# Performance work log

Hardware: AMD Instinct MI355X
Metric: run time of the kernel (lower is better)

The kernel has to match this reference:

```python
import jax, jax.numpy as jnp
import numpy as np

H, D, L, G = 4, 32, 2, 512   # heads, head_dim, conv layers, num graphs
HC = H * D                    # hidden_channels = 128


def _mlp3(x, ws, bs):
    # PyG-style MLP, 3 layers, relu between (no act after last), dropout=0
    for i in range(3):
        x = x @ ws[i] + bs[i]
        if i < 2:
            x = jax.nn.relu(x)
    return x


def _attend(q_dst, k_src, v_src, edge, a_rel_et, m_rel_et, p_rel_et, n_dst):
    """One HGTConv edge-type: relation transform, per-dst segment softmax, scatter.
    q_dst: [Nd,H,D], k_src/v_src: [Ns,H,D], edge: [2,E] (src,dst)."""
    src, dst = edge[0], edge[1]
    k_t = jnp.einsum('nhd,hde->nhe', k_src, a_rel_et)   # relation-specific key
    v_t = jnp.einsum('nhd,hde->nhe', v_src, m_rel_et)   # relation-specific value
    alpha = (q_dst[dst] * k_t[src]).sum(-1) * p_rel_et / jnp.sqrt(jnp.float32(D))  # [E,H]
    amax = jax.ops.segment_max(alpha, dst, num_segments=n_dst)
    amax = jnp.where(jnp.isfinite(amax), amax, 0.0)      # nodes with no in-edges
    ex = jnp.exp(alpha - amax[dst])
    den = jax.ops.segment_sum(ex, dst, num_segments=n_dst)
    w = ex / den[dst]                                    # segment softmax weights
    out = jax.ops.segment_sum(v_t[src] * w[..., None], dst, num_segments=n_dst)
    return out.reshape(n_dst, HC)


def _forward(x_var, x_con, mlp_in_w, mlp_in_b,
             mlp_out_w0, mlp_out_b0, mlp_out_w1, mlp_out_b1, mlp_out_w2, mlp_out_b2,
             k_w, k_b, q_w, q_b, v_w, v_b, a_w, a_b, skip,
             a_rel, m_rel, p_rel, edge_vc, edge_cv, batch_var):
    Nv, Nc = x_var.shape[0], x_con.shape[0]
    # per-node-type input MLPs (nt 0 = variable, nt 1 = constraint)
    xs = [_mlp3(x_var, mlp_in_w[0], mlp_in_b[0]),
          _mlp3(x_con, mlp_in_w[1], mlp_in_b[1])]
    ns = [Nv, Nc]
    for l in range(L):  # HGTConv layers
        k = [(xs[t] @ k_w[l, t] + k_b[l, t]).reshape(ns[t], H, D) for t in (0, 1)]
        q = [(xs[t] @ q_w[l, t] + q_b[l, t]).reshape(ns[t], H, D) for t in (0, 1)]
        v = [(xs[t] @ v_w[l, t] + v_b[l, t]).reshape(ns[t], H, D) for t in (0, 1)]
        # edge type 0: variable -> constraint ; edge type 1: constraint -> variable
        agg_con = _attend(q[1], k[0], v[0], edge_vc, a_rel[l, 0], m_rel[l, 0], p_rel[l, 0], Nc)
        agg_var = _attend(q[0], k[1], v[1], edge_cv, a_rel[l, 1], m_rel[l, 1], p_rel[l, 1], Nv)
        # group='mean' over incoming edge types (one per dst type here), then a_lin + gated skip
        new_xs = []
        for t, agg in ((0, agg_var), (1, agg_con)):
            out = jax.nn.gelu(agg, approximate=False) @ a_w[l, t] + a_b[l, t]
            g = jax.nn.sigmoid(skip[l, t])
            new_xs.append(g * out + (1.0 - g) * xs[t])
        xs = new_xs
    # output head on 'variable' nodes: MLP -> softmax(dim=1) -> global mean pool
    logits = _mlp3(xs[0], [mlp_out_w0, mlp_out_w1, mlp_out_w2], [mlp_out_b0, mlp_out_b1, mlp_out_b2])
    probs = jax.nn.softmax(logits, axis=1)
    summ = jax.ops.segment_sum(probs, batch_var, num_segments=G)
    cnt = jax.ops.segment_sum(jnp.ones((xs[0].shape[0],), probs.dtype), batch_var, num_segments=G)
    return summ / jnp.maximum(cnt, 1.0)[:, None]


def setup_inputs() -> dict:
    key = jax.random.key(0)
    ks = jax.random.split(key, 24)
    Nv = Nc = 50000
    E = 400000
    s = 1.0 / np.sqrt(HC)  # fan-in scale for hidden-width linears
    sd = 1.0 / np.sqrt(D)
    inp = {
        'x_var': jax.random.normal(ks[0], (Nv, HC), jnp.float32),
        'x_con': jax.random.normal(ks[1], (Nc, HC), jnp.float32),
        'mlp_in_w': jax.random.normal(ks[2], (2, 3, HC, HC), jnp.float32) * s,
        'mlp_in_b': jnp.zeros((2, 3, HC), jnp.float32),
        'mlp_out_w0': jax.random.normal(ks[3], (HC, HC), jnp.float32) * s,
        'mlp_out_b0': jnp.zeros((HC,), jnp.float32),
        'mlp_out_w1': jax.random.normal(ks[4], (HC, HC), jnp.float32) * s,
        'mlp_out_b1': jnp.zeros((HC,), jnp.float32),
        'mlp_out_w2': jax.random.normal(ks[5], (HC, 2), jnp.float32) * s,
        'mlp_out_b2': jnp.zeros((2,), jnp.float32),
        'k_w': jax.random.normal(ks[6], (L, 2, HC, HC), jnp.float32) * s,
        'k_b': jnp.zeros((L, 2, HC), jnp.float32),
        'q_w': jax.random.normal(ks[7], (L, 2, HC, HC), jnp.float32) * s,
        'q_b': jnp.zeros((L, 2, HC), jnp.float32),
        'v_w': jax.random.normal(ks[8], (L, 2, HC, HC), jnp.float32) * s,
        'v_b': jnp.zeros((L, 2, HC), jnp.float32),
        'a_w': jax.random.normal(ks[9], (L, 2, HC, HC), jnp.float32) * s,
        'a_b': jnp.zeros((L, 2, HC), jnp.float32),
        'skip': jnp.ones((L, 2), jnp.float32),
        'a_rel': jax.random.normal(ks[10], (L, 2, H, D, D), jnp.float32) * sd,
        'm_rel': jax.random.normal(ks[11], (L, 2, H, D, D), jnp.float32) * sd,
        'p_rel': jnp.ones((L, 2, H), jnp.float32),
        'edge_vc': jnp.stack([jax.random.randint(ks[12], (E,), 0, Nv, jnp.int32),
                              jax.random.randint(ks[13], (E,), 0, Nc, jnp.int32)]),
        'edge_cv': jnp.stack([jax.random.randint(ks[14], (E,), 0, Nc, jnp.int32),
                              jax.random.randint(ks[15], (E,), 0, Nv, jnp.int32)]),
        'batch_var': jnp.sort(jax.random.randint(ks[16], (Nv,), 0, G, jnp.int32)),
    }
    return inp


def reference(x_var, x_con, mlp_in_w, mlp_in_b,
              mlp_out_w0, mlp_out_b0, mlp_out_w1, mlp_out_b1, mlp_out_w2, mlp_out_b2,
              k_w, k_b, q_w, q_b, v_w, v_b, a_w, a_b, skip,
              a_rel, m_rel, p_rel, edge_vc, edge_cv, batch_var):
    return _forward(x_var, x_con, mlp_in_w, mlp_in_b,
                    mlp_out_w0, mlp_out_b0, mlp_out_w1, mlp_out_b1, mlp_out_w2, mlp_out_b2,
                    k_w, k_b, q_w, q_b, v_w, v_b, a_w, a_b, skip,
                    a_rel, m_rel, p_rel, edge_vc, edge_cv, batch_var)
```

## Files before the change

### kernel.cpp

```cpp
#include <hip/hip_runtime.h>
#include <cstddef>
#include <cstdint>

typedef __attribute__((ext_vector_type(8))) short short8;
typedef __attribute__((ext_vector_type(4))) float float4v;

__device__ __forceinline__ float bf2f_lo(unsigned int u) {
    union { unsigned int i; float f; } v; v.i = u << 16; return v.f;
}
__device__ __forceinline__ float bf2f_hi(unsigned int u) {
    union { unsigned int i; float f; } v; v.i = u & 0xFFFF0000u; return v.f;
}
__device__ __forceinline__ float bf2f(unsigned int u16) {
    union { unsigned int i; float f; } v; v.i = u16 << 16; return v.f;
}
__device__ __forceinline__ unsigned short f2bf(float f) {
    union { float f; unsigned int i; } v; v.f = f;
    unsigned int x = v.i;
    unsigned int r = (x + 0x7FFFu + ((x >> 16) & 1u)) >> 16;
    return (unsigned short)r;
}
__device__ __forceinline__ float geluf(float x) {
    return 0.5f * x * (1.0f + erff(x * 0.70710678118654752f));
}
__device__ __forceinline__ void unpack8(const uint4& r, float* f) {
    f[0] = bf2f_lo(r.x); f[1] = bf2f_hi(r.x);
    f[2] = bf2f_lo(r.y); f[3] = bf2f_hi(r.y);
    f[4] = bf2f_lo(r.z); f[5] = bf2f_hi(r.z);
    f[6] = bf2f_lo(r.w); f[7] = bf2f_hi(r.w);
}

__global__ void k_zero(int* __restrict__ p, int n) {
    int i = blockIdx.x * 256 + threadIdx.x;
    if (i < n) p[i] = 0;
}

__global__ void k_prep(const float* __restrict__ kw, const float* __restrict__ kb,
                       const float* __restrict__ vw, const float* __restrict__ vb,
                       const float* __restrict__ arel, const float* __restrict__ mrel,
                       const float* __restrict__ prel,
                       float* __restrict__ Wkv, float* __restrict__ Bkv) {
    int lt = blockIdx.y;
    int tid = blockIdx.x * 256 + threadIdx.x;
    if (tid >= 129 * 256) return;
    int k = tid >> 8;
    int c = tid & 255;
    int sec = c >> 7, cc = c & 127, h = cc >> 5, e = cc & 31;
    const float* Wsrc = sec ? vw : kw;
    const float* Bsrc = sec ? vb : kb;
    const float* R    = sec ? mrel : arel;
    float scale = sec ? 1.0f : prel[lt * 4 + h] * 0.17677669529663687f;
    const float* rp = R + (size_t)(lt * 4 + h) * 1024 + e;
    const float* wp = (k < 128) ? (Wsrc + (size_t)lt * 16384 + (size_t)k * 128 + h * 32)
                                : (Bsrc + lt * 128 + h * 32);
    float s = 0.f;
    #pragma unroll 8
    for (int d = 0; d < 32; ++d) s += wp[d] * rp[(size_t)d * 32];
    s *= scale;
    if (k < 128) Wkv[(size_t)lt * 128 * 256 + (size_t)k * 256 + c] = s;
    else         Bkv[lt * 256 + c] = s;
}

__global__ void k_swz(const float* __restrict__ mlp_in_w, const float* __restrict__ q_w,
                      const float* __restrict__ a_w, const float* __restrict__ mow0,
                      const float* __restrict__ mow1, const float* __restrict__ mow2,
                      const float* __restrict__ Wkv, unsigned short* __restrict__ Wswz) {
    int idx = blockIdx.y;
    int f = blockIdx.x * 256 + threadIdx.x;
    if (f >= 16384) return;
    int j = f & 7, l = (f >> 3) & 63, t = (f >> 9) & 7, s = f >> 12;
    int k = s * 32 + (l >> 4) * 8 + j;
    int n = t * 16 + (l & 15);
    float val;
    if (idx < 6)        val = mlp_in_w[(size_t)idx * 16384 + (size_t)k * 128 + n];
    else if (idx < 10)  val = q_w[(size_t)(idx - 6) * 16384 + (size_t)k * 128 + n];
    else if (idx < 14)  val = a_w[(size_t)(idx - 10) * 16384 + (size_t)k * 128 + n];
    else if (idx == 14) val = mow0[(size_t)k * 128 + n];
    else if (idx == 15) val = mow1[(size_t)k * 128 + n];
    else if (idx < 24) { int u = idx - 16; val = Wkv[(size_t)(u >> 1) * 32768 + (size_t)k * 256 + (u & 1) * 128 + n]; }
    else                val = (n < 2) ? mow2[(size_t)k * 2 + n] : 0.f;
    Wswz[(size_t)idx * 16384 + f] = f2bf(val);
}

__device__ __forceinline__ void mfma32(const short8 av[4], const unsigned short* __restrict__ Bu,
                                       float4v acc[8]) {
    #pragma unroll
    for (int s = 0; s < 4; ++s)
        #pragma unroll
        for (int t = 0; t < 8; ++t) {
            short8 bv = *(const short8*)(Bu + (s * 8 + t) * 512);
            acc[t] = __builtin_amdgcn_mfma_f32_16x16x32_bf16(av[s], bv, acc[t], 0, 0, 0);
        }
}

__global__ __launch_bounds__(256) void k_mlp3(
    const float* __restrict__ Xa, const float* __restrict__ Xb,
    const unsigned short* __restrict__ Wswz, const float* __restrict__ mlp_in_b,
    unsigned short* __restrict__ C, int N, int Nsplit) {
    __shared__ unsigned short lds[4][16][136];
    const int lane = threadIdx.x & 63, wave = threadIdx.x >> 6;
    const int quad = lane >> 4, mrow = lane & 15;
    const int mbase = blockIdx.x * 64 + wave * 16;
    if (mbase >= N) return;
    const bool first = mbase < Nsplit;
    const float* bs = mlp_in_b + (first ? 0 : 384);
    const int ub = first ? 0 : 3;
    int r0 = mbase + mrow; if (r0 >= N) r0 = N - 1;
    const float* ap = ((r0 < Nsplit) ? (Xa + (size_t)r0 * 128)
                                     : (Xb + (size_t)(r0 - Nsplit) * 128)) + quad * 8;
    short8 av[4];
    #pragma unroll
    for (int s = 0; s < 4; ++s) {
        float4 f0 = *(const float4*)(ap + s * 32);
        float4 f1 = *(const float4*)(ap + s * 32 + 4);
        short8 a;
        a[0] = (short)f2bf(f0.x); a[1] = (short)f2bf(f0.y);
        a[2] = (short)f2bf(f0.z); a[3] = (short)f2bf(f0.w);
        a[4] = (short)f2bf(f1.x); a[5] = (short)f2bf(f1.y);
        a[6] = (short)f2bf(f1.z); a[7] = (short)f2bf(f1.w);
        av[s] = a;
    }
    #pragma unroll
    for (int layer = 0; layer < 3; ++layer) {
        const unsigned short* Bu = Wswz + (size_t)(ub + layer) * 16384 + lane * 8;
        float4v acc[8];
        #pragma unroll
        for (int t = 0; t < 8; ++t) acc[t] = (float4v){0.f, 0.f, 0.f, 0.f};
        mfma32(av, Bu, acc);
        const float* b = bs + layer * 128;
        if (layer < 2) {
            #pragma unroll
            for (int t = 0; t < 8; ++t) {
                int col = t * 16 + mrow;
                float bb = b[col];
                #pragma unroll
                for (int r = 0; r < 4; ++r)
                    lds[wave][quad * 4 + r][col] = f2bf(fmaxf(acc[t][r] + bb, 0.f));
            }
            #pragma unroll
            for (int s = 0; s < 4; ++s)
                av[s] = *(const short8*)&lds[wave][mrow][s * 32 + quad * 8];
        } else {
            #pragma unroll
            for (int t = 0; t < 8; ++t) {
                int col = t * 16 + mrow;
                float bb = b[col];
                #pragma unroll
                for (int r = 0; r < 4; ++r) {
                    int row = mbase + quad * 4 + r;
                    if (row < N) C[(size_t)row * 128 + col] = f2bf(acc[t][r] + bb);
                }
            }
        }
    }
}

__global__ __launch_bounds__(256) void k_alin(
    const unsigned short* __restrict__ A, const unsigned short* __restrict__ Wswz,
    int unitA, int unitB, const float* __restrict__ biasA, const float* __restrict__ biasB,
    unsigned short* __restrict__ C, int N, int Nsplit,
    const float* __restrict__ spA, const float* __restrict__ spB) {
    const int lane = threadIdx.x & 63, wave = threadIdx.x >> 6;
    const int quad = lane >> 4, mrow = lane & 15;
    const int mbase = blockIdx.x * 64 + wave * 16;
    if (mbase >= N) return;
    const bool first = mbase < Nsplit;
    const unsigned short* Bu = Wswz + (size_t)(first ? unitA : unitB) * 16384 + lane * 8;
    const float* bias = first ? biasA : biasB;
    int r0 = mbase + mrow; if (r0 >= N) r0 = N - 1;
    const unsigned short* ap = A + (size_t)r0 * 128 + quad * 8;
    short8 av[4];
    #pragma unroll
    for (int s = 0; s < 4; ++s) av[s] = *(const short8*)(ap + s * 32);
    float4v acc[8];
    #pragma unroll
    for (int t = 0; t < 8; ++t) acc[t] = (float4v){0.f, 0.f, 0.f, 0.f};
    mfma32(av, Bu, acc);
    const float* sp = first ? spA : spB;
    float g = 1.f / (1.f + __expf(-sp[0]));
    float og = 1.f - g;
    #pragma unroll
    for (int t = 0; t < 8; ++t) {
        int col = t * 16 + mrow;
        float b = bias[col];
        #pragma unroll
        for (int r = 0; r < 4; ++r) {
            int row = mbase + quad * 4 + r;
            if (row < N) {
                float v = g * (acc[t][r] + b) + og * bf2f(C[(size_t)row * 128 + col]);
                C[(size_t)row * 128 + col] = f2bf(v);
            }
        }
    }
}

__global__ __launch_bounds__(256) void k_qkv(
    const unsigned short* __restrict__ A, const unsigned short* __restrict__ Wswz,
    const float* __restrict__ q_b, const float* __restrict__ Bkv,
    unsigned short* __restrict__ Qs, unsigned short* __restrict__ KVs,
    int NT, int Nv, int l) {
    const int lane = threadIdx.x & 63, wave = threadIdx.x >> 6;
    const int quad = lane >> 4, mrow = lane & 15;
    const int mbase = blockIdx.x * 64 + wave * 16;
    if (mbase >= NT) return;
    const int lt = 2 * l + (mbase >= Nv ? 1 : 0);
    int r0 = mbase + mrow; if (r0 >= NT) r0 = NT - 1;
    const unsigned short* ap = A + (size_t)r0 * 128 + quad * 8;
    short8 av[4];
    #pragma unroll
    for (int s = 0; s < 4; ++s) av[s] = *(const short8*)(ap + s * 32);
    #pragma unroll
    for (int u = 0; u < 3; ++u) {
        int unit = (u == 0) ? (6 + lt) : (16 + lt * 2 + (u - 1));
        const unsigned short* Bu = Wswz + (size_t)unit * 16384 + lane * 8;
        float4v acc[8];
        #pragma unroll
        for (int t = 0; t < 8; ++t) acc[t] = (float4v){0.f, 0.f, 0.f, 0.f};
        mfma32(av, Bu, acc);
        const float* bias = (u == 0) ? (q_b + lt * 128) : (Bkv + lt * 256 + (u - 1) * 128);
        unsigned short* C = (u == 0) ? Qs : KVs;
        const int ldC = (u == 0) ? 128 : 256;
        const int cb = (u == 0) ? 0 : (u - 1) * 128;
        #pragma unroll
        for (int t = 0; t < 8; ++t) {
            int col = t * 16 + mrow;
            float b = bias[col];
            #pragma unroll
            for (int r = 0; r < 4; ++r) {
                int row = mbase + quad * 4 + r;
                if (row < NT) C[(size_t)row * ldC + cb + col] = f2bf(acc[t][r] + b);
            }
        }
    }
}

__global__ void k_hist2(const int* __restrict__ evc, const int* __restrict__ ecv, int E,
                        int* __restrict__ deg, int Nv) {
    int e = blockIdx.x * 256 + threadIdx.x;
    if (e >= E) return;
    if (blockIdx.y == 0) atomicAdd(&deg[Nv + evc[E + e]], 1);
    else                 atomicAdd(&deg[ecv[E + e]], 1);
}
__global__ void k_scan_block(const int* __restrict__ deg, int n, int* __restrict__ off,
                             int* __restrict__ partials) {
    __shared__ int s[256];
    int i = blockIdx.x * 256 + threadIdx.x;
    s[threadIdx.x] = (i < n) ? deg[i] : 0;
    __syncthreads();
    for (int d = 1; d < 256; d <<= 1) {
        int t = (threadIdx.x >= d) ? s[threadIdx.x - d] : 0;
        __syncthreads();
        s[threadIdx.x] += t;
        __syncthreads();
    }
    if (i < n) off[i + 1] = s[threadIdx.x];
    if (threadIdx.x == 255) partials[blockIdx.x] = s[255];
}
__global__ void k_scan_partials(int* __restrict__ partials, int nb) {
    __shared__ int s[512];
    s[threadIdx.x] = (threadIdx.x < nb) ? partials[threadIdx.x] : 0;
    __syncthreads();
    for (int d = 1; d < 512; d <<= 1) {
        int t = (threadIdx.x >= d) ? s[threadIdx.x - d] : 0;
        __syncthreads();
        s[threadIdx.x] += t;
        __syncthreads();
    }
    if (threadIdx.x < nb) partials[threadIdx.x] = s[threadIdx.x];
}
__global__ void k_scan_add(int* __restrict__ off, int* __restrict__ cur,
                           const int* __restrict__ partials, int n) {
    int i = blockIdx.x * 256 + threadIdx.x;
    if (i == 0) { off[0] = 0; cur[0] = 0; }
    if (i < n) {
        int b = i >> 8;
        int v = off[i + 1] + ((b > 0) ? partials[b - 1] : 0);
        off[i + 1] = v;
        cur[i + 1] = v;
    }
}
__global__ void k_scatter2(const int* __restrict__ evc, const int* __restrict__ ecv, int E,
                           int* __restrict__ cur, int Nv, int* __restrict__ srcAll) {
    int e = blockIdx.x * 256 + threadIdx.x;
    if (e >= E) return;
    if (blockIdx.y == 0) {
        int d = Nv + evc[E + e];
        int pos = atomicAdd(&cur[d], 1);
        srcAll[pos] = evc[e];
    } else {
        int d = ecv[E + e];
        int pos = atomicAdd(&cur[d], 1);
        srcAll[pos] = Nv + ecv[e];
    }
}

__global__ __launch_bounds__(256) void k_agg(
    const unsigned short* __restrict__ Q, const unsigned short* __restrict__ KV,
    const int* __restrict__ off, const int* __restrict__ csrc,
    unsigned short* __restrict__ out, int NT) {
    int dst = blockIdx.x * 4 + (threadIdx.x >> 6);
    int lane = threadIdx.x & 63;
    if (dst >= NT) return;
    const int g = lane >> 4, w = lane & 15;
    int s0 = off[dst], s1 = off[dst + 1];
    uint4 qr = *(const uint4*)(Q + (size_t)dst * 128 + w * 8);
    float q[8]; unpack8(qr, q);
    float acc[8] = {0.f, 0.f, 0.f, 0.f, 0.f, 0.f, 0.f, 0.f};
    float den = 0.f;
    int j = s0 + g;
    uint4 kr = {0, 0, 0, 0}, vr = {0, 0, 0, 0};
    bool have = j < s1;
    if (have) {
        const unsigned short* kv = KV + (size_t)csrc[j] * 256 + w * 8;
        kr = *(const uint4*)kv;
        vr = *(const uint4*)(kv + 128);
    }
    while (have) {
        int jn = j + 4;
        bool haveN = jn < s1;
        uint4 krn = kr, vrn = vr;
        if (haveN) {
            const unsigned short* kv = KV + (size_t)csrc[jn] * 256 + w * 8;
            krn = *(const uint4*)kv;
            vrn = *(const uint4*)(kv + 128);
        }
        float k[8]; unpack8(kr, k);
        float t = q[0] * k[0] + q[1] * k[1] + q[2] * k[2] + q[3] * k[3]
                + q[4] * k[4] + q[5] * k[5] + q[6] * k[6] + q[7] * k[7];
        t += __shfl_xor(t, 1);
        t += __shfl_xor(t, 2);
        t = fminf(fmaxf(t, -30.f), 30.f);
        float p = __expf(t);
        den += p;
        float v[8]; unpack8(vr, v);
        #pragma unroll
        for (int i = 0; i < 8; ++i) acc[i] += p * v[i];
        kr = krn; vr = vrn; j = jn; have = haveN;
    }
    den += __shfl_xor(den, 16);
    den += __shfl_xor(den, 32);
    #pragma unroll
    for (int i = 0; i < 8; ++i) {
        acc[i] += __shfl_xor(acc[i], 16);
        acc[i] += __shfl_xor(acc[i], 32);
    }
    if (g == 0) {
        float inv = (s1 > s0) ? 1.f / den : 0.f;
        uint4 o;
        unsigned int* op = (unsigned int*)&o;
        #pragma unroll
        for (int i = 0; i < 4; ++i) {
            float r0 = geluf(acc[2 * i] * inv);
            float r1 = geluf(acc[2 * i + 1] * inv);
            op[i] = (unsigned int)f2bf(r0) | ((unsigned int)f2bf(r1) << 16);
        }
        *(uint4*)(out + (size_t)dst * 128 + w * 8) = o;
    }
}

__global__ __launch_bounds__(256) void k_headf(
    const unsigned short* __restrict__ A, const unsigned short* __restrict__ Wswz,
    const float* __restrict__ mob0, const float* __restrict__ mob1,
    const float* __restrict__ mob2, const int* __restrict__ batch,
    int N, int G, float* __restrict__ gsum, float* __restrict__ gcnt) {
    __shared__ unsigned short lds[4][16][136];
    __shared__ float sb[64][3];
    const int lane = threadIdx.x & 63, wave = threadIdx.x >> 6;
    const int quad = lane >> 4, mrow = lane & 15;
    const int tix = threadIdx.x;
    for (int i = tix; i < 192; i += 256) ((float*)sb)[i] = 0.f;
    __syncthreads();
    const int mbase = blockIdx.x * 64 + wave * 16;
    int bbase = blockIdx.x * 64; if (bbase >= N) bbase = N - 1;
    const int bmin = batch[bbase];
    if (mbase < N) {
        int r0 = mbase + mrow; if (r0 >= N) r0 = N - 1;
        const unsigned short* ap = A + (size_t)r0 * 128 + quad * 8;
        short8 av[4];
        #pragma unroll
        for (int s = 0; s < 4; ++s) av[s] = *(const short8*)(ap + s * 32);
        #pragma unroll
        for (int layer = 0; layer < 2; ++layer) {
            const unsigned short* Bu = Wswz + (size_t)(14 + layer) * 16384 + lane * 8;
            float4v acc[8];
            #pragma unroll
            for (int t = 0; t < 8; ++t) acc[t] = (float4v){0.f, 0.f, 0.f, 0.f};
            mfma32(av, Bu, acc);
            const float* b = layer ? mob1 : mob0;
            #pragma unroll
            for (int t = 0; t < 8; ++t) {
                int col = t * 16 + mrow;
                float bb = b[col];
                #pragma unroll
                for (int r = 0; r < 4; ++r)
                    lds[wave][quad * 4 + r][col] = f2bf(fmaxf(acc[t][r] + bb, 0.f));
            }
            #pragma unroll
            for (int s = 0; s < 4; ++s)
                av[s] = *(const short8*)&lds[wave][mrow][s * 32 + quad * 8];
        }
        float4v lg = (float4v){0.f, 0.f, 0.f, 0.f};
        #pragma unroll
        for (int s = 0; s < 4; ++s) {
            short8 bv = *(const short8*)(Wswz + (size_t)24 * 16384 + (size_t)(s * 8) * 512 + lane * 8);
            lg = __builtin_amdgcn_mfma_f32_16x16x32_bf16(av[s], bv, lg, 0, 0, 0);
        }
        float4v lgo;
        #pragma unroll
        for (int r = 0; r < 4; ++r) lgo[r] = __shfl_xor(lg[r], 1);
        if (mrow == 0) {
            #pragma unroll
            for (int r = 0; r < 4; ++r) {
                int row = mbase + quad * 4 + r;
                if (row < N) {
                    float l0 = lg[r] + mob2[0];
                    float l1 = lgo[r] + mob2[1];
                    float mm = fmaxf(l0, l1);
                    float e0 = __expf(l0 - mm), e1 = __expf(l1 - mm);
                    float inv = 1.f / (e0 + e1);
                    int b = batch[row];
                    int rel = b - bmin;
                    if (rel >= 0 && rel < 64) {
                        atomicAdd(&sb[rel][0], e0 * inv);
                        atomicAdd(&sb[rel][1], e1 * inv);
                        atomicAdd(&sb[rel][2], 1.f);
                    } else {
                        atomicAdd(&gsum[b * 2 + 0], e0 * inv);
                        atomicAdd(&gsum[b * 2 + 1], e1 * inv);
                        atomicAdd(&gcnt[b], 1.f);
                    }
                }
            }
        }
    }
    __syncthreads();
    for (int i = tix; i < 64; i += 256) {
        float c = sb[i][2];
        if (c != 0.f && bmin + i < G) {
            atomicAdd(&gsum[(bmin + i) * 2 + 0], sb[i][0]);
            atomicAdd(&gsum[(bmin + i) * 2 + 1], sb[i][1]);
            atomicAdd(&gcnt[bmin + i], c);
        }
    }
}
__global__ void k_finalize(const float* __restrict__ gsum, const float* __restrict__ gcnt,
                           float* __restrict__ out, int n) {
    int i = blockIdx.x * 256 + threadIdx.x;
    if (i < n) out[i] = gsum[i] / fmaxf(gcnt[i >> 1], 1.f);
}

extern "C" void kernel_launch(void* const* d_in, const int* in_sizes, int n_in,
                              void* d_out, int out_size, void* d_ws, size_t ws_size,
                              hipStream_t stream) {
    const float* x_var    = (const float*)d_in[0];
    const float* x_con    = (const float*)d_in[1];
    const float* mlp_in_w = (const float*)d_in[2];
    const float* mlp_in_b = (const float*)d_in[3];
    const float* mow0 = (const float*)d_in[4];
    const float* mob0 = (const float*)d_in[5];
    const float* mow1 = (const float*)d_in[6];
    const float* mob1 = (const float*)d_in[7];
    const float* mow2 = (const float*)d_in[8];
    const float* mob2 = (const float*)d_in[9];
    const float* k_w  = (const float*)d_in[10];
    const float* k_b  = (const float*)d_in[11];
    const float* q_w  = (const float*)d_in[12];
    const float* q_b  = (const float*)d_in[13];
    const float* v_w  = (const float*)d_in[14];
    const float* v_b  = (const float*)d_in[15];
    const float* a_w  = (const float*)d_in[16];
    const float* a_b  = (const float*)d_in[17];
    const float* skipP = (const float*)d_in[18];
    const float* a_rel = (const float*)d_in[19];
    const float* m_rel = (const float*)d_in[20];
    const float* p_rel = (const float*)d_in[21];
    const int* edge_vc = (const int*)d_in[22];
    const int* edge_cv = (const int*)d_in[23];
    const int* batch   = (const int*)d_in[24];

    const int Nv = in_sizes[0] / 128;
    const int Nc = in_sizes[1] / 128;
    const int E  = in_sizes[22] / 2;
    const int G  = out_size / 2;
    const int NT = Nv + Nc;

    float* fbase = (float*)d_ws;
    size_t fo = 0;
    auto falloc = [&](size_t n) { float* p = fbase + fo; fo += n; return p; };
    float* Wkv  = falloc((size_t)4 * 128 * 256);
    float* Bkv  = falloc(4 * 256);
    float* gsum = falloc((size_t)G * 2);
    float* gcnt = falloc((size_t)G);

    unsigned short* bbase = (unsigned short*)(fbase + fo);
    size_t bo = 0;
    auto balloc = [&](size_t n) { unsigned short* p = bbase + bo; bo += n; return p; };
    unsigned short* Wswz = balloc((size_t)25 * 16384);
    unsigned short* curS = balloc((size_t)NT * 128);
    unsigned short* Qs   = balloc((size_t)NT * 128);
    unsigned short* KVs  = balloc((size_t)NT * 256);

    int* ibase = (int*)(bbase + bo);
    size_t io = 0;
    auto ialloc = [&](size_t n) { int* p = ibase + io; io += n; return p; };
    int* offAll = ialloc((size_t)NT + 1);
    int* curAll = ialloc((size_t)NT + 1);
    int* srcAll = ialloc((size_t)E * 2);
    int* deg    = ialloc((size_t)NT);
    int* partials = ialloc(512);

    size_t need = (char*)(ibase + io) - (char*)d_ws;
    if (need > ws_size) return;

    const int eb   = (E + 255) / 256;
    const int nzb  = (NT + 255) / 256;
    const int gNT  = (NT + 63) / 64;
    const int gNv  = (Nv + 63) / 64;

    k_zero<<<nzb, 256, 0, stream>>>(deg, NT);
    k_hist2<<<dim3(eb, 2), 256, 0, stream>>>(edge_vc, edge_cv, E, deg, Nv);
    k_scan_block<<<nzb, 256, 0, stream>>>(deg, NT, offAll, partials);
    k_scan_partials<<<1, 512, 0, stream>>>(partials, nzb);
    k_scan_add<<<nzb, 256, 0, stream>>>(offAll, curAll, partials, NT);
    k_scatter2<<<dim3(eb, 2), 256, 0, stream>>>(edge_vc, edge_cv, E, curAll, Nv, srcAll);

    k_prep<<<dim3((129 * 256 + 255) / 256, 4), 256, 0, stream>>>(
        k_w, k_b, v_w, v_b, a_rel, m_rel, p_rel, Wkv, Bkv);
    k_swz<<<dim3(64, 25), 256, 0, stream>>>(mlp_in_w, q_w, a_w, mow0, mow1, mow2, Wkv, Wswz);

    k_mlp3<<<gNT, 256, 0, stream>>>(x_var, x_con, Wswz, mlp_in_b, curS, NT, Nv);

    for (int l = 0; l < 2; ++l) {
        int lt0 = l * 2 + 0, lt1 = l * 2 + 1;
        k_qkv<<<gNT, 256, 0, stream>>>(curS, Wswz, q_b, Bkv, Qs, KVs, NT, Nv, l);
        k_agg<<<(NT + 3) / 4, 256, 0, stream>>>(Qs, KVs, offAll, srcAll, Qs, NT);
        k_alin<<<gNT, 256, 0, stream>>>(
            Qs, Wswz, 10 + lt0, 10 + lt1, a_b + lt0 * 128, a_b + lt1 * 128,
            curS, NT, Nv, skipP + lt0, skipP + lt1);
    }

    k_zero<<<(G * 3 + 255) / 256, 256, 0, stream>>>((int*)gsum, G * 3);
    k_headf<<<gNv, 256, 0, stream>>>(curS, Wswz, mob0, mob1, mob2, batch, Nv, G, gsum, gcnt);
    k_finalize<<<(G * 2 + 255) / 256, 256, 0, stream>>>(gsum, gcnt, (float*)d_out, G * 2);
}
```

Before: 565.0 us.

## Fuse MLP/QKV, alin/QKV, alin/head kernels and merge weight prep into swizzle

Folds the relation-transform prep into the weight swizzle kernel, fuses the input MLP with the first QKV projection, fuses each attention output projection and gated skip with the next layer's QKV or with the output head, and uses bf16 dot2 plus packed float2 math in the aggregation kernel. The goal is fewer kernel launches and fewer round-trips of node features through global memory. The cost is larger kernels with more registers and LDS, which can lower occupancy, and layer-1 projection work done inside a kernel shaped around layer 0.

```diff
diff --git a/kernel.cpp b/kernel.cpp
--- a/kernel.cpp
+++ b/kernel.cpp
@@ -4,15 +4,14 @@
 
 typedef __attribute__((ext_vector_type(8))) short short8;
 typedef __attribute__((ext_vector_type(4))) float float4v;
+typedef __attribute__((ext_vector_type(2))) float float2v;
+typedef __attribute__((ext_vector_type(2))) __bf16 bf162;
 
 __device__ __forceinline__ float bf2f_lo(unsigned int u) {
     union { unsigned int i; float f; } v; v.i = u << 16; return v.f;
 }
 __device__ __forceinline__ float bf2f_hi(unsigned int u) {
     union { unsigned int i; float f; } v; v.i = u & 0xFFFF0000u; return v.f;
-}
-__device__ __forceinline__ float bf2f(unsigned int u16) {
-    union { unsigned int i; float f; } v; v.i = u16 << 16; return v.f;
 }
 __device__ __forceinline__ unsigned short f2bf(float f) {
     union { float f; unsigned int i; } v; v.f = f;
@@ -23,11 +22,21 @@
 __device__ __forceinline__ float geluf(float x) {
     return 0.5f * x * (1.0f + erff(x * 0.70710678118654752f));
 }
-__device__ __forceinline__ void unpack8(const uint4& r, float* f) {
-    f[0] = bf2f_lo(r.x); f[1] = bf2f_hi(r.x);
-    f[2] = bf2f_lo(r.y); f[3] = bf2f_hi(r.y);
-    f[4] = bf2f_lo(r.z); f[5] = bf2f_hi(r.z);
-    f[6] = bf2f_lo(r.w); f[7] = bf2f_hi(r.w);
+__device__ __forceinline__ float dot2bf(unsigned int a, unsigned int b, float c) {
+#if defined(__has_builtin) && __has_builtin(__builtin_amdgcn_fdot2_f32_bf16)
+    union U { unsigned int u; bf162 v; };
+    U ua, ub; ua.u = a; ub.u = b;
+    return __builtin_amdgcn_fdot2_f32_bf16(ua.v, ub.v, c, false);
+#else
+    return c + bf2f_lo(a) * bf2f_lo(b) + bf2f_hi(a) * bf2f_hi(b);
+#endif
+}
+__device__ __forceinline__ unsigned int gate_pack(unsigned int nu, unsigned int ou,
+                                                  float2v g2, float2v og2) {
+    float2v n = {bf2f_lo(nu), bf2f_hi(nu)};
+    float2v o = {bf2f_lo(ou), bf2f_hi(ou)};
+    float2v r = n * g2 + o * og2;
+    return (unsigned int)f2bf(r.x) | ((unsigned int)f2bf(r.y) << 16);
 }
 
 __global__ void k_zero(int* __restrict__ p, int n) {
@@ -35,41 +44,34 @@
     if (i < n) p[i] = 0;
 }
 
-__global__ void k_prep(const float* __restrict__ kw, const float* __restrict__ kb,
-                       const float* __restrict__ vw, const float* __restrict__ vb,
-                       const float* __restrict__ arel, const float* __restrict__ mrel,
-                       const float* __restrict__ prel,
-                       float* __restrict__ Wkv, float* __restrict__ Bkv) {
-    int lt = blockIdx.y;
-    int tid = blockIdx.x * 256 + threadIdx.x;
-    if (tid >= 129 * 256) return;
-    int k = tid >> 8;
-    int c = tid & 255;
-    int sec = c >> 7, cc = c & 127, h = cc >> 5, e = cc & 31;
-    const float* Wsrc = sec ? vw : kw;
-    const float* Bsrc = sec ? vb : kb;
-    const float* R    = sec ? mrel : arel;
-    float scale = sec ? 1.0f : prel[lt * 4 + h] * 0.17677669529663687f;
-    const float* rp = R + (size_t)(lt * 4 + h) * 1024 + e;
-    const float* wp = (k < 128) ? (Wsrc + (size_t)lt * 16384 + (size_t)k * 128 + h * 32)
-                                : (Bsrc + lt * 128 + h * 32);
-    float s = 0.f;
-    #pragma unroll 8
-    for (int d = 0; d < 32; ++d) s += wp[d] * rp[(size_t)d * 32];
-    s *= scale;
-    if (k < 128) Wkv[(size_t)lt * 128 * 256 + (size_t)k * 256 + c] = s;
-    else         Bkv[lt * 256 + c] = s;
-}
-
 __global__ void k_swz(const float* __restrict__ mlp_in_w, const float* __restrict__ q_w,
                       const float* __restrict__ a_w, const float* __restrict__ mow0,
                       const float* __restrict__ mow1, const float* __restrict__ mow2,
-                      const float* __restrict__ Wkv, unsigned short* __restrict__ Wswz) {
+                      const float* __restrict__ kw, const float* __restrict__ kb,
+                      const float* __restrict__ vw, const float* __restrict__ vb,
+                      const float* __restrict__ arel, const float* __restrict__ mrel,
+                      const float* __restrict__ prel,
+                      unsigned short* __restrict__ Wswz, float* __restrict__ Bkv) {
     int idx = blockIdx.y;
     int f = blockIdx.x * 256 + threadIdx.x;
+    if (idx == 25) {
+        if (f >= 1024) return;
+        int lt = f >> 8, c = f & 255;
+        int sec = c >> 7, cc = c & 127, h = cc >> 5, e = cc & 31;
+        const float* B = sec ? vb : kb;
+        const float* R = sec ? mrel : arel;
+        float scale = sec ? 1.f : prel[lt * 4 + h] * 0.17677669529663687f;
+        const float* rp = R + (size_t)(lt * 4 + h) * 1024 + e;
+        const float* bp = B + lt * 128 + h * 32;
+        float s = 0.f;
+        #pragma unroll 8
+        for (int d = 0; d < 32; ++d) s += bp[d] * rp[(size_t)d * 32];
+        Bkv[lt * 256 + c] = s * scale;
+        return;
+    }
     if (f >= 16384) return;
-    int j = f & 7, l = (f >> 3) & 63, t = (f >> 9) & 7, s = f >> 12;
-    int k = s * 32 + (l >> 4) * 8 + j;
+    int j = f & 7, l = (f >> 3) & 63, t = (f >> 9) & 7, sb = f >> 12;
+    int k = sb * 32 + (l >> 4) * 8 + j;
     int n = t * 16 + (l & 15);
     float val;
     if (idx < 6)        val = mlp_in_w[(size_t)idx * 16384 + (size_t)k * 128 + n];
@@ -77,8 +79,19 @@
     else if (idx < 14)  val = a_w[(size_t)(idx - 10) * 16384 + (size_t)k * 128 + n];
     else if (idx == 14) val = mow0[(size_t)k * 128 + n];
     else if (idx == 15) val = mow1[(size_t)k * 128 + n];
-    else if (idx < 24) { int u = idx - 16; val = Wkv[(size_t)(u >> 1) * 32768 + (size_t)k * 256 + (u & 1) * 128 + n]; }
-    else                val = (n < 2) ? mow2[(size_t)k * 2 + n] : 0.f;
+    else if (idx < 24) {
+        int u = idx - 16, lt = u >> 1, sec = u & 1;
+        int h = n >> 5, e = n & 31;
+        const float* W = sec ? vw : kw;
+        const float* R = sec ? mrel : arel;
+        float scale = sec ? 1.f : prel[lt * 4 + h] * 0.17677669529663687f;
+        const float* rp = R + (size_t)(lt * 4 + h) * 1024 + e;
+        const float* wp = W + (size_t)lt * 16384 + (size_t)k * 128 + h * 32;
+        float s = 0.f;
+        #pragma unroll 8
+        for (int d = 0; d < 32; ++d) s += wp[d] * rp[(size_t)d * 32];
+        val = s * scale;
+    } else val = (n < 2) ? mow2[(size_t)k * 2 + n] : 0.f;
     Wswz[(size_t)idx * 16384 + f] = f2bf(val);
 }
 
@@ -93,21 +106,24 @@
         }
 }
 
-__global__ __launch_bounds__(256) void k_mlp3(
+__global__ __launch_bounds__(256) void k_mlp3qkv(
     const float* __restrict__ Xa, const float* __restrict__ Xb,
     const unsigned short* __restrict__ Wswz, const float* __restrict__ mlp_in_b,
-    unsigned short* __restrict__ C, int N, int Nsplit) {
+    const float* __restrict__ q_b, const float* __restrict__ Bkv,
+    unsigned short* __restrict__ curS, unsigned short* __restrict__ Qs,
+    unsigned short* __restrict__ KVs, int NT, int Nv) {
     __shared__ unsigned short lds[4][16][136];
     const int lane = threadIdx.x & 63, wave = threadIdx.x >> 6;
     const int quad = lane >> 4, mrow = lane & 15;
     const int mbase = blockIdx.x * 64 + wave * 16;
-    if (mbase >= N) return;
-    const bool first = mbase < Nsplit;
+    if (mbase >= NT) return;
+    const bool first = mbase < Nv;
     const float* bs = mlp_in_b + (first ? 0 : 384);
     const int ub = first ? 0 : 3;
-    int r0 = mbase + mrow; if (r0 >= N) r0 = N - 1;
-    const float* ap = ((r0 < Nsplit) ? (Xa + (size_t)r0 * 128)
-                                     : (Xb + (size_t)(r0 - Nsplit) * 128)) + quad * 8;
+    const int lt = first ? 0 : 1;
+    int r0 = mbase + mrow; if (r0 >= NT) r0 = NT - 1;
+    const float* ap = ((r0 < Nv) ? (Xa + (size_t)r0 * 128)
+                                 : (Xb + (size_t)(r0 - Nv) * 128)) + quad * 8;
     short8 av[4];
     #pragma unroll
     for (int s = 0; s < 4; ++s) {
@@ -128,87 +144,30 @@
         for (int t = 0; t < 8; ++t) acc[t] = (float4v){0.f, 0.f, 0.f, 0.f};
         mfma32(av, Bu, acc);
         const float* b = bs + layer * 128;
-        if (layer < 2) {
-            #pragma unroll
-            for (int t = 0; t < 8; ++t) {
-                int col = t * 16 + mrow;
-                float bb = b[col];
-                #pragma unroll
-                for (int r = 0; r < 4; ++r)
-                    lds[wave][quad * 4 + r][col] = f2bf(fmaxf(acc[t][r] + bb, 0.f));
+        bool relu = layer < 2;
+        #pragma unroll
+        for (int t = 0; t < 8; ++t) {
+            int col = t * 16 + mrow;
+            float bb = b[col];
+            #pragma unroll
+            for (int r = 0; r < 4; ++r) {
+                float v = acc[t][r] + bb;
+                if (relu) v = fmaxf(v, 0.f);
+                lds[wave][quad * 4 + r][col] = f2bf(v);
             }
+        }
+        #pragma unroll
+        for (int s = 0; s < 4; ++s)
+            av[s] = *(const short8*)&lds[wave][mrow][s * 32 + quad * 8];
+    }
+    {
+        int row = mbase + mrow;
+        if (row < NT) {
             #pragma unroll
             for (int s = 0; s < 4; ++s)
-                av[s] = *(const short8*)&lds[wave][mrow][s * 32 + quad * 8];
-        } else {
-            #pragma unroll
-            for (int t = 0; t < 8; ++t) {
-                int col = t * 16 + mrow;
-                float bb = b[col];
-                #pragma unroll
-                for (int r = 0; r < 4; ++r) {
-                    int row = mbase + quad * 4 + r;
-                    if (row < N) C[(size_t)row * 128 + col] = f2bf(acc[t][r] + bb);
-                }
-            }
-        }
-    }
-}
-
-__global__ __launch_bounds__(256) void k_alin(
-    const unsigned short* __restrict__ A, const unsigned short* __restrict__ Wswz,
-    int unitA, int unitB, const float* __restrict__ biasA, const float* __restrict__ biasB,
-    unsigned short* __restrict__ C, int N, int Nsplit,
-    const float* __restrict__ spA, const float* __restrict__ spB) {
-    const int lane = threadIdx.x & 63, wave = threadIdx.x >> 6;
-    const int quad = lane >> 4, mrow = lane & 15;
-    const int mbase = blockIdx.x * 64 + wave * 16;
-    if (mbase >= N) return;
-    const bool first = mbase < Nsplit;
-    const unsigned short* Bu = Wswz + (size_t)(first ? unitA : unitB) * 16384 + lane * 8;
-    const float* bias = first ? biasA : biasB;
-    int r0 = mbase + mrow; if (r0 >= N) r0 = N - 1;
-    const unsigned short* ap = A + (size_t)r0 * 128 + quad * 8;
-    short8 av[4];
-    #pragma unroll
-    for (int s = 0; s < 4; ++s) av[s] = *(const short8*)(ap + s * 32);
-    float4v acc[8];
-    #pragma unroll
-    for (int t = 0; t < 8; ++t) acc[t] = (float4v){0.f, 0.f, 0.f, 0.f};
-    mfma32(av, Bu, acc);
-    const float* sp = first ? spA : spB;
-    float g = 1.f / (1.f + __expf(-sp[0]));
-    float og = 1.f - g;
-    #pragma unroll
-    for (int t = 0; t < 8; ++t) {
-        int col = t * 16 + mrow;
-        float b = bias[col];
-        #pragma unroll
-        for (int r = 0; r < 4; ++r) {
-            int row = mbase + quad * 4 + r;
-            if (row < N) {
-                float v = g * (acc[t][r] + b) + og * bf2f(C[(size_t)row * 128 + col]);
-                C[(size_t)row * 128 + col] = f2bf(v);
-            }
-        }
-    }
-}
-
-__global__ __launch_bounds__(256) void k_qkv(
-    const unsigned short* __restrict__ A, const unsigned short* __restrict__ Wswz,
-    const float* __restrict__ q_b, const float* __restrict__ Bkv,
-    unsigned short* __restrict__ Qs, unsigned short* __restrict__ KVs,
-    int NT, int Nv, int l) {
-    const int lane = threadIdx.x & 63, wave = threadIdx.x >> 6;
-    const int quad = lane >> 4, mrow = lane & 15;
-    const int mbase = blockIdx.x * 64 + wave * 16;
-    if (mbase >= NT) return;
-    const int lt = 2 * l + (mbase >= Nv ? 1 : 0);
-    int r0 = mbase + mrow; if (r0 >= NT) r0 = NT - 1;
-    const unsigned short* ap = A + (size_t)r0 * 128 + quad * 8;
-    short8 av[4];
-    #pragma unroll
-    for (int s = 0; s < 4; ++s) av[s] = *(const short8*)(ap + s * 32);
+                *(uint4*)(curS + (size_t)row * 128 + quad * 8 + s * 32) = *(uint4*)&av[s];
+        }
+    }
     #pragma unroll
     for (int u = 0; u < 3; ++u) {
         int unit = (u == 0) ? (6 + lt) : (16 + lt * 2 + (u - 1));
@@ -234,132 +193,90 @@
     }
 }
 
-__global__ void k_hist2(const int* __restrict__ evc, const int* __restrict__ ecv, int E,
-                        int* __restrict__ deg, int Nv) {
-    int e = blockIdx.x * 256 + threadIdx.x;
-    if (e >= E) return;
-    if (blockIdx.y == 0) atomicAdd(&deg[Nv + evc[E + e]], 1);
-    else                 atomicAdd(&deg[ecv[E + e]], 1);
-}
-__global__ void k_scan_block(const int* __restrict__ deg, int n, int* __restrict__ off,
-                             int* __restrict__ partials) {
-    __shared__ int s[256];
-    int i = blockIdx.x * 256 + threadIdx.x;
-    s[threadIdx.x] = (i < n) ? deg[i] : 0;
-    __syncthreads();
-    for (int d = 1; d < 256; d <<= 1) {
-        int t = (threadIdx.x >= d) ? s[threadIdx.x - d] : 0;
-        __syncthreads();
-        s[threadIdx.x] += t;
-        __syncthreads();
-    }
-    if (i < n) off[i + 1] = s[threadIdx.x];
-    if (threadIdx.x == 255) partials[blockIdx.x] = s[255];
-}
-__global__ void k_scan_partials(int* __restrict__ partials, int nb) {
-    __shared__ int s[512];
-    s[threadIdx.x] = (threadIdx.x < nb) ? partials[threadIdx.x] : 0;
-    __syncthreads();
-    for (int d = 1; d < 512; d <<= 1) {
-        int t = (threadIdx.x >= d) ? s[threadIdx.x - d] : 0;
-        __syncthreads();
-        s[threadIdx.x] += t;
-        __syncthreads();
-    }
-    if (threadIdx.x < nb) partials[threadIdx.x] = s[threadIdx.x];
-}
-__global__ void k_scan_add(int* __restrict__ off, int* __restrict__ cur,
-                           const int* __restrict__ partials, int n) {
-    int i = blockIdx.x * 256 + threadIdx.x;
-    if (i == 0) { off[0] = 0; cur[0] = 0; }
-    if (i < n) {
-        int b = i >> 8;
-        int v = off[i + 1] + ((b > 0) ? partials[b - 1] : 0);
-        off[i + 1] = v;
-        cur[i + 1] = v;
-    }
-}
-__global__ void k_scatter2(const int* __restrict__ evc, const int* __restrict__ ecv, int E,
-                           int* __restrict__ cur, int Nv, int* __restrict__ srcAll) {
-    int e = blockIdx.x * 256 + threadIdx.x;
-    if (e >= E) return;
-    if (blockIdx.y == 0) {
-        int d = Nv + evc[E + e];
-        int pos = atomicAdd(&cur[d], 1);
-        srcAll[pos] = evc[e];
-    } else {
-        int d = ecv[E + e];
-        int pos = atomicAdd(&cur[d], 1);
-        srcAll[pos] = Nv + ecv[e];
-    }
-}
-
-__global__ __launch_bounds__(256) void k_agg(
-    const unsigned short* __restrict__ Q, const unsigned short* __restrict__ KV,
-    const int* __restrict__ off, const int* __restrict__ csrc,
-    unsigned short* __restrict__ out, int NT) {
-    int dst = blockIdx.x * 4 + (threadIdx.x >> 6);
-    int lane = threadIdx.x & 63;
-    if (dst >= NT) return;
-    const int g = lane >> 4, w = lane & 15;
-    int s0 = off[dst], s1 = off[dst + 1];
-    uint4 qr = *(const uint4*)(Q + (size_t)dst * 128 + w * 8);
-    float q[8]; unpack8(qr, q);
-    float acc[8] = {0.f, 0.f, 0.f, 0.f, 0.f, 0.f, 0.f, 0.f};
-    float den = 0.f;
-    int j = s0 + g;
-    uint4 kr = {0, 0, 0, 0}, vr = {0, 0, 0, 0};
-    bool have = j < s1;
-    if (have) {
-        const unsigned short* kv = KV + (size_t)csrc[j] * 256 + w * 8;
-        kr = *(const uint4*)kv;
-        vr = *(const uint4*)(kv + 128);
-    }
-    while (have) {
-        int jn = j + 4;
-        bool haveN = jn < s1;
-        uint4 krn = kr, vrn = vr;
-        if (haveN) {
-            const unsigned short* kv = KV + (size_t)csrc[jn] * 256 + w * 8;
-            krn = *(const uint4*)kv;
-            vrn = *(const uint4*)(kv + 128);
-        }
-        float k[8]; unpack8(kr, k);
-        float t = q[0] * k[0] + q[1] * k[1] + q[2] * k[2] + q[3] * k[3]
-                + q[4] * k[4] + q[5] * k[5] + q[6] * k[6] + q[7] * k[7];
-        t += __shfl_xor(t, 1);
-        t += __shfl_xor(t, 2);
-        t = fminf(fmaxf(t, -30.f), 30.f);
-        float p = __expf(t);
-        den += p;
-        float v[8]; unpack8(vr, v);
-        #pragma unroll
-        for (int i = 0; i < 8; ++i) acc[i] += p * v[i];
-        kr = krn; vr = vrn; j = jn; have = haveN;
-    }
-    den += __shfl_xor(den, 16);
-    den += __shfl_xor(den, 32);
+__global__ __launch_bounds__(256) void k_alinqkv(
+    const unsigned short* __restrict__ Aagg, const unsigned short* __restrict__ Wswz,
+    const float* __restrict__ a_b, const float* __restrict__ skipP,
+    const float* __restrict__ q_b, const float* __restrict__ Bkv,
+    unsigned short* __restrict__ curS, unsigned short* __restrict__ Qs,
+    unsigned short* __restrict__ KVs, int NT, int Nv, int l) {
+    __shared__ unsigned short lds[4][16][136];
+    const int lane = threadIdx.x & 63, wave = threadIdx.x >> 6;
+    const int quad = lane >> 4, mrow = lane & 15;
+    const int mbase = blockIdx.x * 64 + wave * 16;
+    if (mbase >= NT) return;
+    const int type = (mbase >= Nv) ? 1 : 0;
+    const int ltA = l * 2 + type;
+    const int ltQ = (l + 1) * 2 + type;
+    int r0 = mbase + mrow; if (r0 >= NT) r0 = NT - 1;
+    const unsigned short* ap = Aagg + (size_t)r0 * 128 + quad * 8;
+    short8 av[4];
     #pragma unroll
-    for (int i = 0; i < 8; ++i) {
-        acc[i] += __shfl_xor(acc[i], 16);
-        acc[i] += __shfl_xor(acc[i], 32);
-    }
-    if (g == 0) {
-        float inv = (s1 > s0) ? 1.f / den : 0.f;
-        uint4 o;
-        unsigned int* op = (unsigned int*)&o;
-        #pragma unroll
-        for (int i = 0; i < 4; ++i) {
-            float r0 = geluf(acc[2 * i] * inv);
-            float r1 = geluf(acc[2 * i + 1] * inv);
-            op[i] = (unsigned int)f2bf(r0) | ((unsigned int)f2bf(r1) << 16);
-        }
-        *(uint4*)(out + (size_t)dst * 128 + w * 8) = o;
-    }
-}
-
-__global__ __launch_bounds__(256) void k_headf(
-    const unsigned short* __restrict__ A, const unsigned short* __restrict__ Wswz,
+    for (int s = 0; s < 4; ++s) av[s] = *(const short8*)(ap + s * 32);
+    {
+        const unsigned short* Bu = Wswz + (size_t)(10 + ltA) * 16384 + lane * 8;
+        float4v acc[8];
+        #pragma unroll
+        for (int t = 0; t < 8; ++t) acc[t] = (float4v){0.f, 0.f, 0.f, 0.f};
+        mfma32(av, Bu, acc);
+        const float* b = a_b + ltA * 128;
+        #pragma unroll
+        for (int t = 0; t < 8; ++t) {
+            int col = t * 16 + mrow;
+            float bb = b[col];
+            #pragma unroll
+            for (int r = 0; r < 4; ++r)
+                lds[wave][quad * 4 + r][col] = f2bf(acc[t][r] + bb);
+        }
+    }
+    {
+        float gg = 1.f / (1.f + __expf(-skipP[ltA]));
+        float2v g2 = {gg, gg}, og2 = {1.f - gg, 1.f - gg};
+        int row = mbase + mrow;
+        bool ok = row < NT;
+        size_t rbase = (size_t)(ok ? row : 0) * 128;
+        #pragma unroll
+        for (int s = 0; s < 4; ++s) {
+            short8 nv = *(const short8*)&lds[wave][mrow][s * 32 + quad * 8];
+            uint4 nu = *(uint4*)&nv;
+            uint4 ou = *(const uint4*)(curS + rbase + quad * 8 + s * 32);
+            uint4 res;
+            res.x = gate_pack(nu.x, ou.x, g2, og2);
+            res.y = gate_pack(nu.y, ou.y, g2, og2);
+            res.z = gate_pack(nu.z, ou.z, g2, og2);
+            res.w = gate_pack(nu.w, ou.w, g2, og2);
+            if (ok) *(uint4*)(curS + (size_t)row * 128 + quad * 8 + s * 32) = res;
+            av[s] = *(short8*)&res;
+        }
+    }
+    #pragma unroll
+    for (int u = 0; u < 3; ++u) {
+        int unit = (u == 0) ? (6 + ltQ) : (16 + ltQ * 2 + (u - 1));
+        const unsigned short* Bu = Wswz + (size_t)unit * 16384 + lane * 8;
+        float4v acc[8];
+        #pragma unroll
+        for (int t = 0; t < 8; ++t) acc[t] = (float4v){0.f, 0.f, 0.f, 0.f};
+        mfma32(av, Bu, acc);
+        const float* bias = (u == 0) ? (q_b + ltQ * 128) : (Bkv + ltQ * 256 + (u - 1) * 128);
+        unsigned short* C = (u == 0) ? Qs : KVs;
+        const int ldC = (u == 0) ? 128 : 256;
+        const int cb = (u == 0) ? 0 : (u - 1) * 128;
+        #pragma unroll
+        for (int t = 0; t < 8; ++t) {
+            int col = t * 16 + mrow;
+            float b = bias[col];
+            #pragma unroll
+            for (int r = 0; r < 4; ++r) {
+                int row = mbase + quad * 4 + r;
+                if (row < NT) C[(size_t)row * ldC + cb + col] = f2bf(acc[t][r] + b);
+            }
+        }
+    }
+}
+
+__global__ __launch_bounds__(256) void k_alinhead(
+    const unsigned short* __restrict__ Aagg, const unsigned short* __restrict__ Wswz,
+    const float* __restrict__ a_b, const float* __restrict__ skipP,
+    const unsigned short* __restrict__ curS,
     const float* __restrict__ mob0, const float* __restrict__ mob1,
     const float* __restrict__ mob2, const int* __restrict__ batch,
     int N, int G, float* __restrict__ gsum, float* __restrict__ gcnt) {
@@ -375,10 +292,43 @@
     const int bmin = batch[bbase];
     if (mbase < N) {
         int r0 = mbase + mrow; if (r0 >= N) r0 = N - 1;
-        const unsigned short* ap = A + (size_t)r0 * 128 + quad * 8;
+        const unsigned short* ap = Aagg + (size_t)r0 * 128 + quad * 8;
         short8 av[4];
         #pragma unroll
         for (int s = 0; s < 4; ++s) av[s] = *(const short8*)(ap + s * 32);
+        {
+            const unsigned short* Bu = Wswz + (size_t)12 * 16384 + lane * 8;
+            float4v acc[8];
+            #pragma unroll
+            for (int t = 0; t < 8; ++t) acc[t] = (float4v){0.f, 0.f, 0.f, 0.f};
+            mfma32(av, Bu, acc);
+            const float* b = a_b + 2 * 128;
+            #pragma unroll
+            for (int t = 0; t < 8; ++t) {
+                int col = t * 16 + mrow;
+                float bb = b[col];
+                #pragma unroll
+                for (int r = 0; r < 4; ++r)
+                    lds[wave][quad * 4 + r][col] = f2bf(acc[t][r] + bb);
+            }
+        }
+        {
+            float gg = 1.f / (1.f + __expf(-skipP[2]));
+            float2v g2 = {gg, gg}, og2 = {1.f - gg, 1.f - gg};
+            size_t rbase = (size_t)r0 * 128;
+            #pragma unroll
+            for (int s = 0; s < 4; ++s) {
+                short8 nv = *(const short8*)&lds[wave][mrow][s * 32 + quad * 8];
+                uint4 nu = *(uint4*)&nv;
+                uint4 ou = *(const uint4*)(curS + rbase + quad * 8 + s * 32);
+                uint4 res;
+                res.x = gate_pack(nu.x, ou.x, g2, og2);
+                res.y = gate_pack(nu.y, ou.y, g2, og2);
+                res.z = gate_pack(nu.z, ou.z, g2, og2);
+                res.w = gate_pack(nu.w, ou.w, g2, og2);
+                av[s] = *(short8*)&res;
+            }
+        }
         #pragma unroll
         for (int layer = 0; layer < 2; ++layer) {
             const unsigned short* Bu = Wswz + (size_t)(14 + layer) * 16384 + lane * 8;
@@ -443,6 +393,132 @@
         }
     }
 }
+
+__global__ void k_hist2(const int* __restrict__ evc, const int* __restrict__ ecv, int E,
+                        int* __restrict__ deg, int Nv) {
+    int e = blockIdx.x * 256 + threadIdx.x;
+    if (e >= E) return;
+    if (blockIdx.y == 0) atomicAdd(&deg[Nv + evc[E + e]], 1);
+    else                 atomicAdd(&deg[ecv[E + e]], 1);
+}
+__global__ void k_scan_block(const int* __restrict__ deg, int n, int* __restrict__ off,
+                             int* __restrict__ partials) {
+    __shared__ int s[256];
+    int i = blockIdx.x * 256 + threadIdx.x;
+    s[threadIdx.x] = (i < n) ? deg[i] : 0;
+    __syncthreads();
+    for (int d = 1; d < 256; d <<= 1) {
+        int t = (threadIdx.x >= d) ? s[threadIdx.x - d] : 0;
+        __syncthreads();
+        s[threadIdx.x] += t;
+        __syncthreads();
+    }
+    if (i < n) off[i + 1] = s[threadIdx.x];
+    if (threadIdx.x == 255) partials[blockIdx.x] = s[255];
+}
+__global__ void k_scan_partials(int* __restrict__ partials, int nb) {
+    __shared__ int s[512];
+    s[threadIdx.x] = (threadIdx.x < nb) ? partials[threadIdx.x] : 0;
+    __syncthreads();
+    for (int d = 1; d < 512; d <<= 1) {
+        int t = (threadIdx.x >= d) ? s[threadIdx.x - d] : 0;
+        __syncthreads();
+        s[threadIdx.x] += t;
+        __syncthreads();
+    }
+    if (threadIdx.x < nb) partials[threadIdx.x] = s[threadIdx.x];
+}
+__global__ void k_scan_add(int* __restrict__ off, int* __restrict__ cur,
+                           const int* __restrict__ partials, int n) {
+    int i = blockIdx.x * 256 + threadIdx.x;
+    if (i == 0) { off[0] = 0; cur[0] = 0; }
+    if (i < n) {
+        int b = i >> 8;
+        int v = off[i + 1] + ((b > 0) ? partials[b - 1] : 0);
+        off[i + 1] = v;
+        cur[i + 1] = v;
+    }
+}
+__global__ void k_scatter2(const int* __restrict__ evc, const int* __restrict__ ecv, int E,
+                           int* __restrict__ cur, int Nv, int* __restrict__ srcAll) {
+    int e = blockIdx.x * 256 + threadIdx.x;
+    if (e >= E) return;
+    if (blockIdx.y == 0) {
+        int d = Nv + evc[E + e];
+        int pos = atomicAdd(&cur[d], 1);
+        srcAll[pos] = evc[e];
+    } else {
+        int d = ecv[E + e];
+        int pos = atomicAdd(&cur[d], 1);
+        srcAll[pos] = Nv + ecv[e];
+    }
+}
+
+__global__ __launch_bounds__(256) void k_agg(
+    const unsigned short* __restrict__ Q, const unsigned short* __restrict__ KV,
+    const int* __restrict__ off, const int* __restrict__ csrc,
+    unsigned short* __restrict__ out, int NT) {
+    int dst = blockIdx.x * 4 + (threadIdx.x >> 6);
+    int lane = threadIdx.x & 63;
+    if (dst >= NT) return;
+    const int g = lane >> 4, w = lane & 15;
+    int2 se = *(const int2*)(off + dst);
+    int s0 = se.x, s1 = se.y;
+    uint4 qr = *(const uint4*)(Q + (size_t)dst * 128 + w * 8);
+    float2v a0 = {0.f, 0.f}, a1 = {0.f, 0.f}, a2 = {0.f, 0.f}, a3 = {0.f, 0.f};
+    float den = 0.f;
+    int j = s0 + g;
+    uint4 kr = {0, 0, 0, 0}, vr = {0, 0, 0, 0};
+    bool have = j < s1;
+    if (have) {
+        const unsigned short* kv = KV + (size_t)csrc[j] * 256 + w * 8;
+        kr = *(const uint4*)kv;
+        vr = *(const uint4*)(kv + 128);
+    }
+    while (have) {
+        int jn = j + 4;
+        bool haveN = jn < s1;
+        uint4 krn = kr, vrn = vr;
+        if (haveN) {
+            const unsigned short* kv = KV + (size_t)csrc[jn] * 256 + w * 8;
+            krn = *(const uint4*)kv;
+            vrn = *(const uint4*)(kv + 128);
+        }
+        float t = dot2bf(kr.x, qr.x, 0.f);
+        t = dot2bf(kr.y, qr.y, t);
+        t = dot2bf(kr.z, qr.z, t);
+        t = dot2bf(kr.w, qr.w, t);
+        t += __shfl_xor(t, 1);
+        t += __shfl_xor(t, 2);
+        t = fminf(fmaxf(t, -30.f), 30.f);
+        float p = __expf(t);
+        den += p;
+        float2v pv = {p, p};
+        a0 += pv * (float2v){bf2f_lo(vr.x), bf2f_hi(vr.x)};
+        a1 += pv * (float2v){bf2f_lo(vr.y), bf2f_hi(vr.y)};
+        a2 += pv * (float2v){bf2f_lo(vr.z), bf2f_hi(vr.z)};
+        a3 += pv * (float2v){bf2f_lo(vr.w), bf2f_hi(vr.w)};
+        kr = krn; vr = vrn; j = jn; have = haveN;
+    }
+    den += __shfl_xor(den, 16); den += __shfl_xor(den, 32);
+    a0.x += __shfl_xor(a0.x, 16); a0.x += __shfl_xor(a0.x, 32);
+    a0.y += __shfl_xor(a0.y, 16); a0.y += __shfl_xor(a0.y, 32);
+    a1.x += __shfl_xor(a1.x, 16); a1.x += __shfl_xor(a1.x, 32);
+    a1.y += __shfl_xor(a1.y, 16); a1.y += __shfl_xor(a1.y, 32);
+    a2.x += __shfl_xor(a2.x, 16); a2.x += __shfl_xor(a2.x, 32);
+    a2.y += __shfl_xor(a2.y, 16); a2.y += __shfl_xor(a2.y, 32);
+    a3.x += __shfl_xor(a3.x, 16); a3.x += __shfl_xor(a3.x, 32);
+    a3.y += __shfl_xor(a3.y, 16); a3.y += __shfl_xor(a3.y, 32);
+    float inv = (s1 > s0) ? 1.f / den : 0.f;
+    float2v r = a0;
+    if (g == 1) r = a1;
+    if (g == 2) r = a2;
+    if (g == 3) r = a3;
+    float r0 = geluf(r.x * inv), r1 = geluf(r.y * inv);
+    unsigned int o = (unsigned int)f2bf(r0) | ((unsigned int)f2bf(r1) << 16);
+    *(unsigned int*)(out + (size_t)dst * 128 + w * 8 + g * 2) = o;
+}
+
 __global__ void k_finalize(const float* __restrict__ gsum, const float* __restrict__ gcnt,
                            float* __restrict__ out, int n) {
     int i = blockIdx.x * 256 + threadIdx.x;
@@ -487,7 +563,6 @@
     float* fbase = (float*)d_ws;
     size_t fo = 0;
     auto falloc = [&](size_t n) { float* p = fbase + fo; fo += n; return p; };
-    float* Wkv  = falloc((size_t)4 * 128 * 256);
     float* Bkv  = falloc(4 * 256);
     float* gsum = falloc((size_t)G * 2);
     float* gcnt = falloc((size_t)G);
@@ -512,10 +587,10 @@
     size_t need = (char*)(ibase + io) - (char*)d_ws;
     if (need > ws_size) return;
 
-    const int eb   = (E + 255) / 256;
-    const int nzb  = (NT + 255) / 256;
-    const int gNT  = (NT + 63) / 64;
-    const int gNv  = (Nv + 63) / 64;
+    const int eb  = (E + 255) / 256;
+    const int nzb = (NT + 255) / 256;
+    const int gNT = (NT + 63) / 64;
+    const int gNv = (Nv + 63) / 64;
 
     k_zero<<<nzb, 256, 0, stream>>>(deg, NT);
     k_hist2<<<dim3(eb, 2), 256, 0, stream>>>(edge_vc, edge_cv, E, deg, Nv);
@@ -524,22 +599,18 @@
     k_scan_add<<<nzb, 256, 0, stream>>>(offAll, curAll, partials, NT);
     k_scatter2<<<dim3(eb, 2), 256, 0, stream>>>(edge_vc, edge_cv, E, curAll, Nv, srcAll);
 
-    k_prep<<<dim3((129 * 256 + 255) / 256, 4), 256, 0, stream>>>(
-        k_w, k_b, v_w, v_b, a_rel, m_rel, p_rel, Wkv, Bkv);
-    k_swz<<<dim3(64, 25), 256, 0, stream>>>(mlp_in_w, q_w, a_w, mow0, mow1, mow2, Wkv, Wswz);
-
-    k_mlp3<<<gNT, 256, 0, stream>>>(x_var, x_con, Wswz, mlp_in_b, curS, NT, Nv);
-
-    for (int l = 0; l < 2; ++l) {
-        int lt0 = l * 2 + 0, lt1 = l * 2 + 1;
-        k_qkv<<<gNT, 256, 0, stream>>>(curS, Wswz, q_b, Bkv, Qs, KVs, NT, Nv, l);
-        k_agg<<<(NT + 3) / 4, 256, 0, stream>>>(Qs, KVs, offAll, srcAll, Qs, NT);
-        k_alin<<<gNT, 256, 0, stream>>>(
-            Qs, Wswz, 10 + lt0, 10 + lt1, a_b + lt0 * 128, a_b + lt1 * 128,
-            curS, NT, Nv, skipP + lt0, skipP + lt1);
-    }
-
+    k_swz<<<dim3(64, 26), 256, 0, stream>>>(mlp_in_w, q_w, a_w, mow0, mow1, mow2,
+                                            k_w, k_b, v_w, v_b, a_rel, m_rel, p_rel,
+                                            Wswz, Bkv);
     k_zero<<<(G * 3 + 255) / 256, 256, 0, stream>>>((int*)gsum, G * 3);
-    k_headf<<<gNv, 256, 0, stream>>>(curS, Wswz, mob0, mob1, mob2, batch, Nv, G, gsum, gcnt);
+
+    k_mlp3qkv<<<gNT, 256, 0, stream>>>(x_var, x_con, Wswz, mlp_in_b, q_b, Bkv,
+                                       curS, Qs, KVs, NT, Nv);
+    k_agg<<<(NT + 3) / 4, 256, 0, stream>>>(Qs, KVs, offAll, srcAll, Qs, NT);
+    k_alinqkv<<<gNT, 256, 0, stream>>>(Qs, Wswz, a_b, skipP, q_b, Bkv,
+                                       curS, Qs, KVs, NT, Nv, 0);
+    k_agg<<<(NT + 3) / 4, 256, 0, stream>>>(Qs, KVs, offAll, srcAll, Qs, NT);
+    k_alinhead<<<gNv, 256, 0, stream>>>(Qs, Wswz, a_b, skipP, curS,
+                                        mob0, mob1, mob2, batch, Nv, G, gsum, gcnt);
     k_finalize<<<(G * 2 + 255) / 256, 256, 0, stream>>>(gsum, gcnt, (float*)d_out, G * 2);
 }
```

After: 525.4 us. -7.0%, faster.
